# Performance work log

Measured on AMD Instinct MI355X. Metric: run time of the kernel, lower is better.

Reference implementation:

```python
import jax, jax.numpy as jnp
import numpy as np

N_NODES = 100000
N_EDGES = 3200000
EPS = 1e-5
NEG_SLOPE = 0.1


def _glorot(key, fan_in, fan_out):
    lim = np.sqrt(6.0 / (fan_in + fan_out))
    return jax.random.uniform(key, (fan_in, fan_out), jnp.float32, -lim, lim)


def setup_inputs() -> dict:
    key = jax.random.key(0)
    ks = jax.random.split(key, 16)
    x = jax.random.normal(ks[0], (N_NODES, 3), jnp.float32)
    edge_index = jax.random.randint(ks[1], (2, N_EDGES), 0, N_NODES, jnp.int32)
    dims = [(3, 64), (64, 64), (64, 256), (256, 256), (256, 512), (512, 1)]
    inp = {"x": x, "edge_index": edge_index}
    for i, (fi, fo) in enumerate(dims):
        inp[f"W{i+1}"] = _glorot(ks[2 + i], fi, fo)
        inp[f"b{i+1}"] = jnp.zeros((fo,), jnp.float32)
    for i, fo in enumerate([64, 64, 256, 256, 512]):
        inp[f"g{i+1}"] = jnp.ones((fo,), jnp.float32)
        inp[f"bt{i+1}"] = jnp.zeros((fo,), jnp.float32)
    return inp


def _gcn_conv(h, W, b, src, dst, dis):
    # transform first (cheaper when out_dim <= in_dim is not guaranteed, but
    # avoids gathering raw features twice); then edge-normalized scatter-add.
    hw = h @ W                                   # [N, Fo]
    norm = dis[src] * dis[dst]                   # [E]
    agg = jax.ops.segment_sum(hw[src] * norm[:, None], dst, num_segments=N_NODES)
    agg = agg + (dis * dis)[:, None] * hw        # self-loop term (norm = dis_i^2)
    return agg + b


def _bn(h, g, bt):
    mu = jnp.mean(h, axis=0)
    var = jnp.mean((h - mu) ** 2, axis=0)        # biased var, as torch BN
    return (h - mu) * jax.lax.rsqrt(var + EPS) * g + bt


def _lrelu(h):
    return jnp.where(h > 0, h, NEG_SLOPE * h)


def reference(x, edge_index, W1, b1, W2, b2, W3, b3, W4, b4, W5, b5, W6, b6,
              g1, bt1, g2, bt2, g3, bt3, g4, bt4, g5, bt5):
    src, dst = edge_index[0], edge_index[1]
    # degree includes the added self-loop (+1), symmetric normalization
    deg = jax.ops.segment_sum(jnp.ones((N_EDGES,), x.dtype), dst,
                              num_segments=N_NODES) + 1.0
    dis = jax.lax.rsqrt(deg)

    h = x
    Ws = [W1, W2, W3, W4, W5]
    bs = [b1, b2, b3, b4, b5]
    gs = [g1, g2, g3, g4, g5]
    bts = [bt1, bt2, bt3, bt4, bt5]
    for W, b, g, bt in zip(Ws, bs, gs, bts):
        h = _gcn_conv(h, W, b, src, dst, dis)
        h = _lrelu(_bn(h, g, bt))
    h = _gcn_conv(h, W6, b6, src, dst, dis)
    return jax.nn.sigmoid(h)
```

## Files before the change

kernel.cpp:

```cpp
#include <hip/hip_runtime.h>
#include <math.h>

typedef unsigned short u16;
typedef unsigned int u32;
typedef __attribute__((ext_vector_type(8))) short bf16x8;
typedef __attribute__((ext_vector_type(4))) float f32x4;

constexpr float EPS_BN = 1e-5f;
constexpr float NEG = 0.1f;
constexpr int LDP = 800;

static inline int cdiv(int a, int b) { return (a + b - 1) / b; }


__device__ __forceinline__ float b2f_lo(u32 v) { return __uint_as_float(v << 16); }
__device__ __forceinline__ float b2f_hi(u32 v) { return __uint_as_float(v & 0xFFFF0000u); }
__device__ __forceinline__ float b2f(u16 v) { return __uint_as_float(((u32)v) << 16); }
__device__ __forceinline__ u16 f2b(float f) {
  u32 u = __float_as_uint(f);
  u32 r = u + 0x7FFFu + ((u >> 16) & 1u);
  return (u16)(r >> 16);
}
__device__ __forceinline__ u32 pack2(float a, float b) {
  return (u32)f2b(a) | ((u32)f2b(b) << 16);
}
__device__ __forceinline__ void unpack8(uint4 v, float* o) {
  o[0] = b2f_lo(v.x); o[1] = b2f_hi(v.x);
  o[2] = b2f_lo(v.y); o[3] = b2f_hi(v.y);
  o[4] = b2f_lo(v.z); o[5] = b2f_hi(v.z);
  o[6] = b2f_lo(v.w); o[7] = b2f_hi(v.w);
}
__device__ __forceinline__ void unpack4(uint2 v, float* o) {
  o[0] = b2f_lo(v.x); o[1] = b2f_hi(v.x);
  o[2] = b2f_lo(v.y); o[3] = b2f_hi(v.y);
}


__global__ void k_zero_i32(int* p, int n) {
  int i = blockIdx.x * blockDim.x + threadIdx.x;
  if (i < n) p[i] = 0;
}

__global__ __launch_bounds__(256) void k_bcount(const int* __restrict__ dst,
                                                int* __restrict__ bucketCnt, int E) {
  __shared__ int hist[256];
  int tid = threadIdx.x;
  hist[tid] = 0;
  __syncthreads();
  int e0 = blockIdx.x * 4096;
#pragma unroll
  for (int i = 0; i < 16; ++i) {
    int e = e0 + i * 256 + tid;
    if (e < E) atomicAdd(&hist[dst[e] >> 9], 1);
  }
  __syncthreads();
  int h = hist[tid];
  if (h > 0) atomicAdd(&bucketCnt[tid], h);
}

__global__ void k_bscan(const int* __restrict__ bucketCnt, int* __restrict__ bucketOff,
                        int* __restrict__ bucketCur, int NB, int E) {
  __shared__ int s[256];
  int tid = threadIdx.x;
  int v = (tid < NB) ? bucketCnt[tid] : 0;
  s[tid] = v;
  __syncthreads();
  for (int off = 1; off < 256; off <<= 1) {
    int t = (tid >= off) ? s[tid - off] : 0;
    __syncthreads();
    s[tid] += t;
    __syncthreads();
  }
  if (tid < NB) bucketOff[tid] = s[tid] - v;
  if (tid == NB) bucketOff[NB] = E;
  if (tid < NB) bucketCur[tid] = 0;
}

__global__ __launch_bounds__(256) void k_bucket(const int* __restrict__ src,
                                                const int* __restrict__ dst,
                                                const int* __restrict__ bucketOff,
                                                int* __restrict__ bucketCur,
                                                u32* __restrict__ ebuf, int E) {
  __shared__ int hist[256];
  __shared__ int base[256];
  __shared__ int lcur[256];
  int tid = threadIdx.x;
  hist[tid] = 0; lcur[tid] = 0;
  __syncthreads();
  int e0 = blockIdx.x * 4096;
  int ss[16], dd[16];
#pragma unroll
  for (int i = 0; i < 16; ++i) {
    int e = e0 + i * 256 + tid;
    if (e < E) {
      ss[i] = src[e]; dd[i] = dst[e];
      atomicAdd(&hist[dd[i] >> 9], 1);
    } else dd[i] = -1;
  }
  __syncthreads();
  int h = hist[tid];
  if (h > 0) base[tid] = bucketOff[tid] + atomicAdd(&bucketCur[tid], h);
  __syncthreads();
#pragma unroll
  for (int i = 0; i < 16; ++i) {
    if (dd[i] >= 0) {
      int bk = dd[i] >> 9;
      int p = atomicAdd(&lcur[bk], 1);
      ebuf[base[bk] + p] = ((u32)ss[i] << 9) | ((u32)dd[i] & 511u);
    }
  }
}

__global__ __launch_bounds__(256) void k_csr(const u32* __restrict__ ebuf,
                                             const int* __restrict__ bucketOff,
                                             int* __restrict__ rowoff,
                                             int* __restrict__ col,
                                             float* __restrict__ dis,
                                             int N, int E, int NB) {
  __shared__ int hist[512];
  __shared__ int loff[512];
  __shared__ int scan_s[256];
  int b = blockIdx.x;
  int tid = threadIdx.x;
  int ebase = bucketOff[b], eend = bucketOff[b + 1];
  int ecnt = eend - ebase;
  hist[tid] = 0; hist[tid + 256] = 0;
  __syncthreads();
  for (int i = tid; i < ecnt; i += 256)
    atomicAdd(&hist[ebuf[ebase + i] & 511u], 1);
  __syncthreads();
  int h0 = hist[2 * tid], h1 = hist[2 * tid + 1];
  int ts = h0 + h1;
  scan_s[tid] = ts;
  __syncthreads();
  for (int off = 1; off < 256; off <<= 1) {
    int t = (tid >= off) ? scan_s[tid - off] : 0;
    __syncthreads();
    scan_s[tid] += t;
    __syncthreads();
  }
  int excl = scan_s[tid] - ts;
  loff[2 * tid] = excl;
  loff[2 * tid + 1] = excl + h0;
  __syncthreads();
  int gbase = b * 512;
  for (int i = tid; i < 512; i += 256) {
    int node = gbase + i;
    if (node < N) {
      rowoff[node] = ebase + loff[i];
      dis[node] = rsqrtf((float)hist[i] + 1.0f);
    }
  }
  if (b == NB - 1 && tid == 0) rowoff[N] = E;
  __syncthreads();
  for (int i = tid; i < ecnt; i += 256) {
    u32 ed = ebuf[ebase + i];
    int p = atomicAdd(&loff[ed & 511u], 1);
    col[ebase + p] = (int)(ed >> 9);
  }
}


__global__ void k_l1(const float* __restrict__ x, const int* __restrict__ rowoff,
                     const int* __restrict__ col, const float* __restrict__ dis,
                     const float* __restrict__ W, const float* __restrict__ b,
                     u16* __restrict__ z, int n) {
  int wid = (blockIdx.x * blockDim.x + threadIdx.x) >> 6;
  int lane = threadIdx.x & 63;
  if (wid >= n) return;
  float a0 = 0.f, a1 = 0.f, a2 = 0.f;
  int beg = rowoff[wid], end = rowoff[wid + 1];
  for (int e = beg + lane; e < end; e += 64) {
    int j = col[e];
    float dj = dis[j];
    a0 += dj * x[j * 3 + 0];
    a1 += dj * x[j * 3 + 1];
    a2 += dj * x[j * 3 + 2];
  }
#pragma unroll
  for (int off = 32; off; off >>= 1) {
    a0 += __shfl_xor(a0, off); a1 += __shfl_xor(a1, off); a2 += __shfl_xor(a2, off);
  }
  float di = dis[wid];
  a0 = di * (a0 + di * x[wid * 3 + 0]);
  a1 = di * (a1 + di * x[wid * 3 + 1]);
  a2 = di * (a2 + di * x[wid * 3 + 2]);
  float zv = a0 * W[lane] + a1 * W[64 + lane] + a2 * W[128 + lane] + b[lane];
  z[(size_t)wid * 64 + lane] = f2b(zv);
}


__global__ void k_agg64(const u16* __restrict__ u, const int* __restrict__ rowoff,
                        const int* __restrict__ col, const float* __restrict__ dis,
                        u16* __restrict__ a, int n) {
  int wid = (blockIdx.x * blockDim.x + threadIdx.x) >> 6;
  int lane = threadIdx.x & 63;
  if (wid >= n) return;
  int sub = lane >> 4, c = lane & 15;
  const uint2* u2 = (const uint2*)u;
  float acc[4] = {0.f, 0.f, 0.f, 0.f};
  if (sub == 0) {
    float s[4]; unpack4(u2[(size_t)wid * 16 + c], s);
#pragma unroll
    for (int k = 0; k < 4; ++k) acc[k] = s[k];
  }
  int beg = rowoff[wid], end = rowoff[wid + 1];
  int e = beg + sub;
  int j1 = (e < end) ? col[e] : -1;
  int j2 = (e + 4 < end) ? col[e + 4] : -1;
  while (j1 >= 0) {
    int en = e + 8;
    int nj1 = -1, nj2 = -1;
    if (j2 >= 0) {
      if (en < end) nj1 = col[en];
      if (en + 4 < end) nj2 = col[en + 4];
    }
    {
      float f1[4]; unpack4(u2[(size_t)j1 * 16 + c], f1);
#pragma unroll
      for (int k = 0; k < 4; ++k) acc[k] += f1[k];
    }
    if (j2 >= 0) {
      float f2[4]; unpack4(u2[(size_t)j2 * 16 + c], f2);
#pragma unroll
      for (int k = 0; k < 4; ++k) acc[k] += f2[k];
    }
    e = en; j1 = nj1; j2 = nj2;
  }
#pragma unroll
  for (int k = 0; k < 4; ++k) {
    acc[k] += __shfl_xor(acc[k], 16);
    acc[k] += __shfl_xor(acc[k], 32);
  }
  if (sub == 0) {
    float d = dis[wid];
    ((uint2*)a)[(size_t)wid * 16 + c] =
        make_uint2(pack2(d * acc[0], d * acc[1]), pack2(d * acc[2], d * acc[3]));
  }
}

__global__ void k_agg256(const u16* __restrict__ u, const int* __restrict__ rowoff,
                         const int* __restrict__ col, const float* __restrict__ dis,
                         u16* __restrict__ a, int n) {
  int wid = (blockIdx.x * blockDim.x + threadIdx.x) >> 6;
  int lane = threadIdx.x & 63;
  if (wid >= n) return;
  int sub = lane >> 5, c = lane & 31;
  const uint4* u4 = (const uint4*)u;
  float acc[8] = {0.f, 0.f, 0.f, 0.f, 0.f, 0.f, 0.f, 0.f};
  if (sub == 0) {
    float s[8]; unpack8(u4[(size_t)wid * 32 + c], s);
#pragma unroll
    for (int k = 0; k < 8; ++k) acc[k] = s[k];
  }
  int beg = rowoff[wid], end = rowoff[wid + 1];
  int e = beg + sub;
  int j1 = (e < end) ? col[e] : -1;
  int j2 = (e + 2 < end) ? col[e + 2] : -1;
  while (j1 >= 0) {
    int en = e + 4;
    int nj1 = -1, nj2 = -1;
    if (j2 >= 0) {
      if (en < end) nj1 = col[en];
      if (en + 2 < end) nj2 = col[en + 2];
    }
    {
      float f1[8]; unpack8(u4[(size_t)j1 * 32 + c], f1);
#pragma unroll
      for (int k = 0; k < 8; ++k) acc[k] += f1[k];
    }
    if (j2 >= 0) {
      float f2[8]; unpack8(u4[(size_t)j2 * 32 + c], f2);
#pragma unroll
      for (int k = 0; k < 8; ++k) acc[k] += f2[k];
    }
    e = en; j1 = nj1; j2 = nj2;
  }
#pragma unroll
  for (int k = 0; k < 8; ++k) acc[k] += __shfl_xor(acc[k], 32);
  if (sub == 0) {
    float d = dis[wid];
    uint4 r;
    r.x = pack2(d * acc[0], d * acc[1]);
    r.y = pack2(d * acc[2], d * acc[3]);
    r.z = pack2(d * acc[4], d * acc[5]);
    r.w = pack2(d * acc[6], d * acc[7]);
    ((uint4*)a)[(size_t)wid * 32 + c] = r;
  }
}


__global__ void k_u(u16* __restrict__ z, const float* __restrict__ scaleF,
                    const float* __restrict__ shiftF, const float* __restrict__ dis,
                    int n, int lg) {
  size_t idx = (size_t)blockIdx.x * blockDim.x + threadIdx.x;
  size_t tot = ((size_t)n) << lg;
  if (idx >= tot) return;
  int g = (int)(idx & ((1u << lg) - 1));
  int node = (int)(idx >> lg);
  uint4 v = ((const uint4*)z)[idx];
  float f[8];
  unpack8(v, f);
  int f0 = g * 8;
  float4 s0 = *(const float4*)&scaleF[f0];
  float4 s1 = *(const float4*)&scaleF[f0 + 4];
  float4 h0 = *(const float4*)&shiftF[f0];
  float4 h1 = *(const float4*)&shiftF[f0 + 4];
  float d = dis[node];
  float o[8];
  o[0] = f[0] * s0.x + h0.x; o[1] = f[1] * s0.y + h0.y;
  o[2] = f[2] * s0.z + h0.z; o[3] = f[3] * s0.w + h0.w;
  o[4] = f[4] * s1.x + h1.x; o[5] = f[5] * s1.y + h1.y;
  o[6] = f[6] * s1.z + h1.z; o[7] = f[7] * s1.w + h1.w;
#pragma unroll
  for (int k = 0; k < 8; ++k) {
    float a = o[k];
    a = (a > 0.f) ? a : NEG * a;
    o[k] = d * a;
  }
  uint4 r;
  r.x = pack2(o[0], o[1]); r.y = pack2(o[2], o[3]);
  r.z = pack2(o[4], o[5]); r.w = pack2(o[6], o[7]);
  ((uint4*)z)[idx] = r;
}


__global__ void k_wt_all(const float* __restrict__ W2, const float* __restrict__ W3,
                         const float* __restrict__ W4, const float* __restrict__ W5,
                         u16* __restrict__ WT) {
  int i = blockIdx.x * blockDim.x + threadIdx.x;
  const float* W; int K, Fo, base;
  if (i < 4096)        { W = W2; K = 64;  Fo = 64;  base = 0; }
  else if (i < 20480)  { W = W3; K = 64;  Fo = 256; base = 4096; }
  else if (i < 86016)  { W = W4; K = 256; Fo = 256; base = 20480; }
  else if (i < 217088) { W = W5; K = 256; Fo = 512; base = 86016; }
  else return;
  int idx = i - base;
  int f = idx / K, k = idx - f * K;
  WT[i] = f2b(W[(size_t)k * Fo + f]);
}


__global__ __launch_bounds__(256) void k_gemm(const u16* __restrict__ A,
                                              const u16* __restrict__ WT,
                                              const float* __restrict__ bias,
                                              u16* __restrict__ C,
                                              float* __restrict__ psum,
                                              float* __restrict__ psq,
                                              int n, int K, int Fo, int nby) {
  __shared__ u16 As[128][72];
  __shared__ u16 Bs[128][72];
  int tid = threadIdx.x;
  int nwg = gridDim.x;
  int bid = blockIdx.x;
  int q = nwg >> 3, rr = nwg & 7;
  int xcd = bid & 7, pos = bid >> 3;
  int wgid = (xcd < rr ? xcd * (q + 1) : rr * (q + 1) + (xcd - rr) * q) + pos;
  int bx = wgid / nby, by = wgid - bx * nby;
  int bm0 = bx * 128, bn0 = by * 128;
  int lane = tid & 63, wid = tid >> 6;
  int wm = wid >> 1, wn = wid & 1;
  int lr = tid & 127;
  int lh = (tid >> 7) * 32;
  int fr = lane & 15, fg = lane >> 4;
  f32x4 acc[4][4];
#pragma unroll
  for (int i = 0; i < 4; ++i)
#pragma unroll
    for (int j = 0; j < 4; ++j) acc[i][j] = (f32x4)0.0f;

  for (int kt = 0; kt < K; kt += 64) {
    {
      int row = bm0 + lr;
      uint4 v[4];
#pragma unroll
      for (int i = 0; i < 4; ++i) {
        v[i] = make_uint4(0u, 0u, 0u, 0u);
        if (row < n) v[i] = *(const uint4*)&A[(size_t)row * K + kt + lh + i * 8];
      }
      int fo = bn0 + lr;
      uint4 w[4];
#pragma unroll
      for (int i = 0; i < 4; ++i) {
        w[i] = make_uint4(0u, 0u, 0u, 0u);
        if (fo < Fo) w[i] = *(const uint4*)&WT[(size_t)fo * K + kt + lh + i * 8];
      }
#pragma unroll
      for (int i = 0; i < 4; ++i) *(uint4*)&As[lr][lh + i * 8] = v[i];
#pragma unroll
      for (int i = 0; i < 4; ++i) *(uint4*)&Bs[lr][lh + i * 8] = w[i];
    }
    __syncthreads();
#pragma unroll
    for (int ks = 0; ks < 2; ++ks) {
      int k0 = ks * 32 + fg * 8;
      bf16x8 af[4], bf[4];
#pragma unroll
      for (int mi = 0; mi < 4; ++mi) af[mi] = *(const bf16x8*)&As[wm * 64 + mi * 16 + fr][k0];
#pragma unroll
      for (int ni = 0; ni < 4; ++ni) bf[ni] = *(const bf16x8*)&Bs[wn * 64 + ni * 16 + fr][k0];
#pragma unroll
      for (int mi = 0; mi < 4; ++mi)
#pragma unroll
        for (int ni = 0; ni < 4; ++ni)
          acc[mi][ni] = __builtin_amdgcn_mfma_f32_16x16x32_bf16(af[mi], bf[ni], acc[mi][ni], 0, 0, 0);
    }
    __syncthreads();
  }
  float* s2 = (float*)&As[0][0];
#pragma unroll
  for (int ni = 0; ni < 4; ++ni) {
    int gc = bn0 + wn * 64 + ni * 16 + fr;
    float ps = 0.f, pq = 0.f;
    if (gc < Fo) {
      float bv = bias[gc];
#pragma unroll
      for (int mi = 0; mi < 4; ++mi) {
#pragma unroll
        for (int rg = 0; rg < 4; ++rg) {
          int gr = bm0 + wm * 64 + mi * 16 + fg * 4 + rg;
          if (gr < n) {
            float v = acc[mi][ni][rg] + bv;
            C[(size_t)gr * Fo + gc] = f2b(v);
            ps += v; pq += v * v;
          }
        }
      }
    }
    ps += __shfl_xor(ps, 16); ps += __shfl_xor(ps, 32);
    pq += __shfl_xor(pq, 16); pq += __shfl_xor(pq, 32);
    if (fg == 0 && gc < Fo) {
      int cl = wn * 64 + ni * 16 + fr;
      s2[wm * 128 + cl] = ps;
      s2[256 + wm * 128 + cl] = pq;
    }
  }
  __syncthreads();
  if (tid < 128) {
    int gc = bn0 + tid;
    if (gc < Fo) {
      psum[(size_t)gc * LDP + bx] = s2[tid] + s2[128 + tid];
      psq[(size_t)gc * LDP + bx] = s2[256 + tid] + s2[384 + tid];
    }
  }
}


__global__ void k_colred(const u16* __restrict__ z, int Fo, int n, int rowsPerChunk,
                         float* __restrict__ psum, float* __restrict__ psq) {
  int fl = threadIdx.x & 63;
  int rg = threadIdx.x >> 6;
  int f = blockIdx.y * 64 + fl;
  int r0 = blockIdx.x * rowsPerChunk;
  int r1 = min(n, r0 + rowsPerChunk);
  float s = 0.f, sq = 0.f;
  for (int r = r0 + rg; r < r1; r += 4) {
    float v = b2f(z[(size_t)r * Fo + f]);
    s += v;
    sq += v * v;
  }
  __shared__ float ls[4][64], lq[4][64];
  ls[rg][fl] = s; lq[rg][fl] = sq;
  __syncthreads();
  if (rg == 0) {
    psum[(size_t)f * LDP + blockIdx.x] = ls[0][fl] + ls[1][fl] + ls[2][fl] + ls[3][fl];
    psq[(size_t)f * LDP + blockIdx.x] = lq[0][fl] + lq[1][fl] + lq[2][fl] + lq[3][fl];
  }
}

__global__ void k_bnparams(const float* __restrict__ psum, const float* __restrict__ psq,
                           int Fo, int nChunks, int n,
                           const float* __restrict__ g, const float* __restrict__ bt,
                           float* __restrict__ scaleF, float* __restrict__ shiftF) {
  int f = blockIdx.x * 4 + (threadIdx.x >> 6);
  int lane = threadIdx.x & 63;
  if (f >= Fo) return;
  float s = 0.f, sq = 0.f;
  const float* ps = &psum[(size_t)f * LDP];
  const float* pq = &psq[(size_t)f * LDP];
  for (int c = lane; c < nChunks; c += 64) { s += ps[c]; sq += pq[c]; }
#pragma unroll
  for (int off = 32; off; off >>= 1) {
    s += __shfl_xor(s, off);
    sq += __shfl_xor(sq, off);
  }
  if (lane == 0) {
    float inv = 1.0f / (float)n;
    float mu = s * inv;
    float var = sq * inv - mu * mu;
    float rs = rsqrtf(var + EPS_BN) * g[f];
    scaleF[f] = rs;
    shiftF[f] = bt[f] - mu * rs;
  }
}


__global__ void k_dot512(const u16* __restrict__ z, const float* __restrict__ scaleF,
                         const float* __restrict__ shiftF, const float* __restrict__ w6,
                         const float* __restrict__ dis, float* __restrict__ v, int n) {
  __shared__ float ws[512], scs[512], shs[512];
  int tid = threadIdx.x;
  for (int i = tid; i < 512; i += 256) { ws[i] = w6[i]; scs[i] = scaleF[i]; shs[i] = shiftF[i]; }
  __syncthreads();
  int lane = tid % 64, wv = tid / 64;
  int node = blockIdx.x * 4 + wv;
  if (node >= n) return;
  uint4 vz = *(const uint4*)&z[(size_t)node * 512 + lane * 8];
  float f[8];
  unpack8(vz, f);
  int f0 = lane * 8;
  float s = 0.f;
#pragma unroll
  for (int k = 0; k < 8; ++k) {
    float a = f[k] * scs[f0 + k] + shs[f0 + k];
    a = (a > 0.f) ? a : NEG * a;
    s += a * ws[f0 + k];
  }
#pragma unroll
  for (int off = 32; off > 0; off >>= 1) s += __shfl_down(s, off);
  if (lane == 0) v[node] = dis[node] * s;
}

__global__ void k_final(const float* __restrict__ v, const int* __restrict__ rowoff,
                        const int* __restrict__ col, const float* __restrict__ dis,
                        const float* __restrict__ b6, float* __restrict__ out, int n) {
  int wid = (blockIdx.x * blockDim.x + threadIdx.x) >> 6;
  int lane = threadIdx.x & 63;
  if (wid >= n) return;
  float acc = 0.f;
  int beg = rowoff[wid], end = rowoff[wid + 1];
  for (int e = beg + lane; e < end; e += 64) acc += v[col[e]];
#pragma unroll
  for (int off = 32; off; off >>= 1) acc += __shfl_xor(acc, off);
  if (lane == 0) {
    float zz = dis[wid] * (acc + v[wid]) + b6[0];
    out[wid] = 1.0f / (1.0f + expf(-zz));
  }
}


extern "C" void kernel_launch(void* const* d_in, const int* in_sizes, int n_in,
                              void* d_out, int out_size, void* d_ws, size_t ws_size,
                              hipStream_t stream) {
  const float* x = (const float*)d_in[0];
  const int* ei = (const int*)d_in[1];
  const int N = in_sizes[0] / 3;
  const int E = in_sizes[1] / 2;
  const int* srcIdx = ei;
  const int* dstIdx = ei + E;

  const float* W[6]; const float* b[6];
  for (int i = 0; i < 6; ++i) { W[i] = (const float*)d_in[2 + 2 * i]; b[i] = (const float*)d_in[3 + 2 * i]; }
  const float* g[5]; const float* bt[5];
  for (int i = 0; i < 5; ++i) { g[i] = (const float*)d_in[14 + 2 * i]; bt[i] = (const float*)d_in[15 + 2 * i]; }

  char* wsB = (char*)d_ws;
  size_t off = 0;
  auto alloc = [&](size_t bytes) -> void* {
    void* p = wsB + off;
    off = (off + bytes + 255) & ~(size_t)255;
    return p;
  };

  const int NB = cdiv(N, 512);
  int* rowoff = (int*)alloc((size_t)(N + 1) * 4);
  int* col = (int*)alloc((size_t)E * 4);
  float* dis = (float*)alloc((size_t)N * 4);
  float* vbuf = (float*)alloc((size_t)N * 4);
  float* scaleF = (float*)alloc(512 * 4);
  float* shiftF = (float*)alloc(512 * 4);
  u16* WTb = (u16*)alloc((size_t)217088 * 2);
  int* bucketCnt = (int*)alloc(256 * 4);
  int* bucketOff = (int*)alloc(257 * 4);
  int* bucketCur = (int*)alloc(256 * 4);
  const int nbx = cdiv(N, 128);
  float* psum = (float*)alloc((size_t)512 * LDP * 4);
  float* psq = (float*)alloc((size_t)512 * LDP * 4);
  u16* Zb = (u16*)alloc((size_t)N * 512 * 2);
  u16* Ab = (u16*)alloc((size_t)N * 256 * 2);
  u32* ebuf = (u32*)Ab;

  const int wtOff[5] = {0, 0, 4096, 20480, 86016};
  k_wt_all<<<cdiv(217088, 256), 256, 0, stream>>>(W[1], W[2], W[3], W[4], WTb);

  const int EB = cdiv(E, 4096);
  k_zero_i32<<<1, 256, 0, stream>>>(bucketCnt, 256);
  k_bcount<<<EB, 256, 0, stream>>>(dstIdx, bucketCnt, E);
  k_bscan<<<1, 256, 0, stream>>>(bucketCnt, bucketOff, bucketCur, NB, E);
  k_bucket<<<EB, 256, 0, stream>>>(srcIdx, dstIdx, bucketOff, bucketCur, ebuf, E);
  k_csr<<<NB, 256, 0, stream>>>(ebuf, bucketOff, rowoff, col, dis, N, E, NB);

  auto gemm = [&](const u16* Ain, int layer, int K, int Fo, u16* Cout) {
    int nby = cdiv(Fo, 128);
    k_gemm<<<nbx * nby, 256, 0, stream>>>(Ain, WTb + wtOff[layer], b[layer], Cout,
                                          psum, psq, N, K, Fo, nby);
    k_bnparams<<<cdiv(Fo, 4), 256, 0, stream>>>(psum, psq, Fo, nbx, N,
                                                g[layer], bt[layer], scaleF, shiftF);
  };

  const int waveGrid = cdiv(N * 64, 256);

  k_l1<<<waveGrid, 256, 0, stream>>>(x, rowoff, col, dis, W[0], b[0], Zb, N);
  {
    const int rowsPerChunk = 2048;
    const int nChunks = cdiv(N, rowsPerChunk);
    dim3 grid(nChunks, 1);
    k_colred<<<grid, 256, 0, stream>>>(Zb, 64, N, rowsPerChunk, psum, psq);
    k_bnparams<<<cdiv(64, 4), 256, 0, stream>>>(psum, psq, 64, nChunks, N, g[0], bt[0], scaleF, shiftF);
  }

  k_u<<<cdiv(N * 8, 256), 256, 0, stream>>>(Zb, scaleF, shiftF, dis, N, 3);
  k_agg64<<<waveGrid, 256, 0, stream>>>(Zb, rowoff, col, dis, Ab, N);
  gemm(Ab, 1, 64, 64, Zb);

  k_u<<<cdiv(N * 8, 256), 256, 0, stream>>>(Zb, scaleF, shiftF, dis, N, 3);
  k_agg64<<<waveGrid, 256, 0, stream>>>(Zb, rowoff, col, dis, Ab, N);
  gemm(Ab, 2, 64, 256, Zb);

  k_u<<<cdiv(N * 32, 256), 256, 0, stream>>>(Zb, scaleF, shiftF, dis, N, 5);
  k_agg256<<<waveGrid, 256, 0, stream>>>(Zb, rowoff, col, dis, Ab, N);
  gemm(Ab, 3, 256, 256, Zb);

  k_u<<<cdiv(N * 32, 256), 256, 0, stream>>>(Zb, scaleF, shiftF, dis, N, 5);
  k_agg256<<<waveGrid, 256, 0, stream>>>(Zb, rowoff, col, dis, Ab, N);
  gemm(Ab, 4, 256, 512, Zb);

  k_dot512<<<cdiv(N, 4), 256, 0, stream>>>(Zb, scaleF, shiftF, W[5], dis, vbuf, N);
  k_final<<<waveGrid, 256, 0, stream>>>(vbuf, rowoff, col, dis, b[5], (float*)d_out, N);
}
```

Measured before the change: 1.235 ms.

## Fuse BN+LeakyReLU into aggregation and use direct-to-LDS swizzled GEMM loads

```diff
diff --git a/kernel.cpp b/kernel.cpp
--- a/kernel.cpp
+++ b/kernel.cpp
@@ -33,6 +33,13 @@
 __device__ __forceinline__ void unpack4(uint2 v, float* o) {
   o[0] = b2f_lo(v.x); o[1] = b2f_hi(v.x);
   o[2] = b2f_lo(v.y); o[3] = b2f_hi(v.y);
+}
+__device__ __forceinline__ float lrelu_s(float t) { return fmaxf(t, NEG * t); }
+
+__device__ __forceinline__ void gload16(const void* g, void* l) {
+  __builtin_amdgcn_global_load_lds(
+      (const __attribute__((address_space(1))) u32*)g,
+      (__attribute__((address_space(3))) u32*)l, 16, 0, 0);
 }
 
 
@@ -190,24 +197,29 @@
 }
 
 
-__global__ void k_agg64(const u16* __restrict__ u, const int* __restrict__ rowoff,
+__global__ void k_agg64(const u16* __restrict__ z, const int* __restrict__ rowoff,
                         const int* __restrict__ col, const float* __restrict__ dis,
+                        const float* __restrict__ scaleF, const float* __restrict__ shiftF,
                         u16* __restrict__ a, int n) {
   int wid = (blockIdx.x * blockDim.x + threadIdx.x) >> 6;
   int lane = threadIdx.x & 63;
   if (wid >= n) return;
   int sub = lane >> 4, c = lane & 15;
-  const uint2* u2 = (const uint2*)u;
+  const uint2* z2 = (const uint2*)z;
+  float sc[4], sh[4];
+  {
+    float4 s = *(const float4*)&scaleF[c * 4];
+    float4 h = *(const float4*)&shiftF[c * 4];
+    sc[0] = s.x; sc[1] = s.y; sc[2] = s.z; sc[3] = s.w;
+    sh[0] = h.x; sh[1] = h.y; sh[2] = h.z; sh[3] = h.w;
+  }
   float acc[4] = {0.f, 0.f, 0.f, 0.f};
-  if (sub == 0) {
-    float s[4]; unpack4(u2[(size_t)wid * 16 + c], s);
-#pragma unroll
-    for (int k = 0; k < 4; ++k) acc[k] = s[k];
-  }
   int beg = rowoff[wid], end = rowoff[wid + 1];
   int e = beg + sub;
   int j1 = (e < end) ? col[e] : -1;
   int j2 = (e + 4 < end) ? col[e + 4] : -1;
+  float d1 = (j1 >= 0) ? dis[j1] : 0.f;
+  float d2 = (j2 >= 0) ? dis[j2] : 0.f;
   while (j1 >= 0) {
     int en = e + 8;
     int nj1 = -1, nj2 = -1;
@@ -215,17 +227,19 @@
       if (en < end) nj1 = col[en];
       if (en + 4 < end) nj2 = col[en + 4];
     }
+    float nd1 = (nj1 >= 0) ? dis[nj1] : 0.f;
+    float nd2 = (nj2 >= 0) ? dis[nj2] : 0.f;
     {
-      float f1[4]; unpack4(u2[(size_t)j1 * 16 + c], f1);
-#pragma unroll
-      for (int k = 0; k < 4; ++k) acc[k] += f1[k];
+      float f1[4]; unpack4(z2[(size_t)j1 * 16 + c], f1);
+#pragma unroll
+      for (int k = 0; k < 4; ++k) acc[k] += lrelu_s(d1 * (f1[k] * sc[k] + sh[k]));
     }
     if (j2 >= 0) {
-      float f2[4]; unpack4(u2[(size_t)j2 * 16 + c], f2);
-#pragma unroll
-      for (int k = 0; k < 4; ++k) acc[k] += f2[k];
-    }
-    e = en; j1 = nj1; j2 = nj2;
+      float f2[4]; unpack4(z2[(size_t)j2 * 16 + c], f2);
+#pragma unroll
+      for (int k = 0; k < 4; ++k) acc[k] += lrelu_s(d2 * (f2[k] * sc[k] + sh[k]));
+    }
+    e = en; j1 = nj1; j2 = nj2; d1 = nd1; d2 = nd2;
   }
 #pragma unroll
   for (int k = 0; k < 4; ++k) {
@@ -233,30 +247,42 @@
     acc[k] += __shfl_xor(acc[k], 32);
   }
   if (sub == 0) {
-    float d = dis[wid];
+    float dw = dis[wid];
+    float s[4]; unpack4(z2[(size_t)wid * 16 + c], s);
+#pragma unroll
+    for (int k = 0; k < 4; ++k) acc[k] = dw * (acc[k] + lrelu_s(dw * (s[k] * sc[k] + sh[k])));
     ((uint2*)a)[(size_t)wid * 16 + c] =
-        make_uint2(pack2(d * acc[0], d * acc[1]), pack2(d * acc[2], d * acc[3]));
-  }
-}
-
-__global__ void k_agg256(const u16* __restrict__ u, const int* __restrict__ rowoff,
+        make_uint2(pack2(acc[0], acc[1]), pack2(acc[2], acc[3]));
+  }
+}
+
+__global__ void k_agg256(const u16* __restrict__ z, const int* __restrict__ rowoff,
                          const int* __restrict__ col, const float* __restrict__ dis,
+                         const float* __restrict__ scaleF, const float* __restrict__ shiftF,
                          u16* __restrict__ a, int n) {
   int wid = (blockIdx.x * blockDim.x + threadIdx.x) >> 6;
   int lane = threadIdx.x & 63;
   if (wid >= n) return;
   int sub = lane >> 5, c = lane & 31;
-  const uint4* u4 = (const uint4*)u;
+  const uint4* z4 = (const uint4*)z;
+  float sc[8], sh[8];
+  {
+    float4 s0 = *(const float4*)&scaleF[c * 8];
+    float4 s1 = *(const float4*)&scaleF[c * 8 + 4];
+    float4 h0 = *(const float4*)&shiftF[c * 8];
+    float4 h1 = *(const float4*)&shiftF[c * 8 + 4];
+    sc[0] = s0.x; sc[1] = s0.y; sc[2] = s0.z; sc[3] = s0.w;
+    sc[4] = s1.x; sc[5] = s1.y; sc[6] = s1.z; sc[7] = s1.w;
+    sh[0] = h0.x; sh[1] = h0.y; sh[2] = h0.z; sh[3] = h0.w;
+    sh[4] = h1.x; sh[5] = h1.y; sh[6] = h1.z; sh[7] = h1.w;
+  }
   float acc[8] = {0.f, 0.f, 0.f, 0.f, 0.f, 0.f, 0.f, 0.f};
-  if (sub == 0) {
-    float s[8]; unpack8(u4[(size_t)wid * 32 + c], s);
-#pragma unroll
-    for (int k = 0; k < 8; ++k) acc[k] = s[k];
-  }
   int beg = rowoff[wid], end = rowoff[wid + 1];
   int e = beg + sub;
   int j1 = (e < end) ? col[e] : -1;
   int j2 = (e + 2 < end) ? col[e + 2] : -1;
+  float d1 = (j1 >= 0) ? dis[j1] : 0.f;
+  float d2 = (j2 >= 0) ? dis[j2] : 0.f;
   while (j1 >= 0) {
     int en = e + 4;
     int nj1 = -1, nj2 = -1;
@@ -264,64 +290,34 @@
       if (en < end) nj1 = col[en];
       if (en + 2 < end) nj2 = col[en + 2];
     }
+    float nd1 = (nj1 >= 0) ? dis[nj1] : 0.f;
+    float nd2 = (nj2 >= 0) ? dis[nj2] : 0.f;
     {
-      float f1[8]; unpack8(u4[(size_t)j1 * 32 + c], f1);
-#pragma unroll
-      for (int k = 0; k < 8; ++k) acc[k] += f1[k];
+      float f1[8]; unpack8(z4[(size_t)j1 * 32 + c], f1);
+#pragma unroll
+      for (int k = 0; k < 8; ++k) acc[k] += lrelu_s(d1 * (f1[k] * sc[k] + sh[k]));
     }
     if (j2 >= 0) {
-      float f2[8]; unpack8(u4[(size_t)j2 * 32 + c], f2);
-#pragma unroll
-      for (int k = 0; k < 8; ++k) acc[k] += f2[k];
-    }
-    e = en; j1 = nj1; j2 = nj2;
+      float f2[8]; unpack8(z4[(size_t)j2 * 32 + c], f2);
+#pragma unroll
+      for (int k = 0; k < 8; ++k) acc[k] += lrelu_s(d2 * (f2[k] * sc[k] + sh[k]));
+    }
+    e = en; j1 = nj1; j2 = nj2; d1 = nd1; d2 = nd2;
   }
 #pragma unroll
   for (int k = 0; k < 8; ++k) acc[k] += __shfl_xor(acc[k], 32);
   if (sub == 0) {
-    float d = dis[wid];
+    float dw = dis[wid];
+    float s[8]; unpack8(z4[(size_t)wid * 32 + c], s);
+#pragma unroll
+    for (int k = 0; k < 8; ++k) acc[k] = dw * (acc[k] + lrelu_s(dw * (s[k] * sc[k] + sh[k])));
     uint4 r;
-    r.x = pack2(d * acc[0], d * acc[1]);
-    r.y = pack2(d * acc[2], d * acc[3]);
-    r.z = pack2(d * acc[4], d * acc[5]);
-    r.w = pack2(d * acc[6], d * acc[7]);
+    r.x = pack2(acc[0], acc[1]);
+    r.y = pack2(acc[2], acc[3]);
+    r.z = pack2(acc[4], acc[5]);
+    r.w = pack2(acc[6], acc[7]);
     ((uint4*)a)[(size_t)wid * 32 + c] = r;
   }
-}
-
-
-__global__ void k_u(u16* __restrict__ z, const float* __restrict__ scaleF,
-                    const float* __restrict__ shiftF, const float* __restrict__ dis,
-                    int n, int lg) {
-  size_t idx = (size_t)blockIdx.x * blockDim.x + threadIdx.x;
-  size_t tot = ((size_t)n) << lg;
-  if (idx >= tot) return;
-  int g = (int)(idx & ((1u << lg) - 1));
-  int node = (int)(idx >> lg);
-  uint4 v = ((const uint4*)z)[idx];
-  float f[8];
-  unpack8(v, f);
-  int f0 = g * 8;
-  float4 s0 = *(const float4*)&scaleF[f0];
-  float4 s1 = *(const float4*)&scaleF[f0 + 4];
-  float4 h0 = *(const float4*)&shiftF[f0];
-  float4 h1 = *(const float4*)&shiftF[f0 + 4];
-  float d = dis[node];
-  float o[8];
-  o[0] = f[0] * s0.x + h0.x; o[1] = f[1] * s0.y + h0.y;
-  o[2] = f[2] * s0.z + h0.z; o[3] = f[3] * s0.w + h0.w;
-  o[4] = f[4] * s1.x + h1.x; o[5] = f[5] * s1.y + h1.y;
-  o[6] = f[6] * s1.z + h1.z; o[7] = f[7] * s1.w + h1.w;
-#pragma unroll
-  for (int k = 0; k < 8; ++k) {
-    float a = o[k];
-    a = (a > 0.f) ? a : NEG * a;
-    o[k] = d * a;
-  }
-  uint4 r;
-  r.x = pack2(o[0], o[1]); r.y = pack2(o[2], o[3]);
-  r.z = pack2(o[4], o[5]); r.w = pack2(o[6], o[7]);
-  ((uint4*)z)[idx] = r;
 }
 
 
@@ -348,8 +344,8 @@
                                               float* __restrict__ psum,
                                               float* __restrict__ psq,
                                               int n, int K, int Fo, int nby) {
-  __shared__ u16 As[128][72];
-  __shared__ u16 Bs[128][72];
+  __shared__ u16 As[128 * 64];
+  __shared__ u16 Bs[128 * 64];
   int tid = threadIdx.x;
   int nwg = gridDim.x;
   int bid = blockIdx.x;
@@ -358,11 +354,11 @@
   int wgid = (xcd < rr ? xcd * (q + 1) : rr * (q + 1) + (xcd - rr) * q) + pos;
   int bx = wgid / nby, by = wgid - bx * nby;
   int bm0 = bx * 128, bn0 = by * 128;
-  int lane = tid & 63, wid = tid >> 6;
-  int wm = wid >> 1, wn = wid & 1;
-  int lr = tid & 127;
-  int lh = (tid >> 7) * 32;
+  int lane = tid & 63, wv = tid >> 6;
+  int wm = wv >> 1, wn = wv & 1;
   int fr = lane & 15, fg = lane >> 4;
+  int srow = lane >> 3;
+  int cb = (lane & 7) ^ srow;
   f32x4 acc[4][4];
 #pragma unroll
   for (int i = 0; i < 4; ++i)
@@ -370,25 +366,13 @@
     for (int j = 0; j < 4; ++j) acc[i][j] = (f32x4)0.0f;
 
   for (int kt = 0; kt < K; kt += 64) {
-    {
-      int row = bm0 + lr;
-      uint4 v[4];
-#pragma unroll
-      for (int i = 0; i < 4; ++i) {
-        v[i] = make_uint4(0u, 0u, 0u, 0u);
-        if (row < n) v[i] = *(const uint4*)&A[(size_t)row * K + kt + lh + i * 8];
-      }
-      int fo = bn0 + lr;
-      uint4 w[4];
-#pragma unroll
-      for (int i = 0; i < 4; ++i) {
-        w[i] = make_uint4(0u, 0u, 0u, 0u);
-        if (fo < Fo) w[i] = *(const uint4*)&WT[(size_t)fo * K + kt + lh + i * 8];
-      }
-#pragma unroll
-      for (int i = 0; i < 4; ++i) *(uint4*)&As[lr][lh + i * 8] = v[i];
-#pragma unroll
-      for (int i = 0; i < 4; ++i) *(uint4*)&Bs[lr][lh + i * 8] = w[i];
+#pragma unroll
+    for (int i = 0; i < 4; ++i) {
+      int rb = 8 * (4 * wv + i);
+      const u16* ga = &A[(size_t)(bm0 + rb + srow) * K + kt + cb * 8];
+      gload16(ga, &As[rb * 64 + lane * 8]);
+      const u16* gb = &WT[(size_t)(bn0 + rb + srow) * K + kt + cb * 8];
+      gload16(gb, &Bs[rb * 64 + lane * 8]);
     }
     __syncthreads();
 #pragma unroll
@@ -396,9 +380,17 @@
       int k0 = ks * 32 + fg * 8;
       bf16x8 af[4], bf[4];
 #pragma unroll
-      for (int mi = 0; mi < 4; ++mi) af[mi] = *(const bf16x8*)&As[wm * 64 + mi * 16 + fr][k0];
-#pragma unroll
-      for (int ni = 0; ni < 4; ++ni) bf[ni] = *(const bf16x8*)&Bs[wn * 64 + ni * 16 + fr][k0];
+      for (int mi = 0; mi < 4; ++mi) {
+        int row = wm * 64 + mi * 16 + fr;
+        int byt = (row * 128 + k0 * 2) ^ ((row & 7) << 4);
+        af[mi] = *(const bf16x8*)((const char*)As + byt);
+      }
+#pragma unroll
+      for (int ni = 0; ni < 4; ++ni) {
+        int row = wn * 64 + ni * 16 + fr;
+        int byt = (row * 128 + k0 * 2) ^ ((row & 7) << 4);
+        bf[ni] = *(const bf16x8*)((const char*)Bs + byt);
+      }
 #pragma unroll
       for (int mi = 0; mi < 4; ++mi)
 #pragma unroll
@@ -407,7 +399,7 @@
     }
     __syncthreads();
   }
-  float* s2 = (float*)&As[0][0];
+  float* s2 = (float*)&As[0];
 #pragma unroll
   for (int ni = 0; ni < 4; ++ni) {
     int gc = bn0 + wn * 64 + ni * 16 + fr;
@@ -577,7 +569,7 @@
   float* psum = (float*)alloc((size_t)512 * LDP * 4);
   float* psq = (float*)alloc((size_t)512 * LDP * 4);
   u16* Zb = (u16*)alloc((size_t)N * 512 * 2);
-  u16* Ab = (u16*)alloc((size_t)N * 256 * 2);
+  u16* Ab = (u16*)alloc((size_t)(N + 128) * 256 * 2);
   u32* ebuf = (u32*)Ab;
 
   const int wtOff[5] = {0, 0, 4096, 20480, 86016};
@@ -609,20 +601,16 @@
     k_bnparams<<<cdiv(64, 4), 256, 0, stream>>>(psum, psq, 64, nChunks, N, g[0], bt[0], scaleF, shiftF);
   }
 
-  k_u<<<cdiv(N * 8, 256), 256, 0, stream>>>(Zb, scaleF, shiftF, dis, N, 3);
-  k_agg64<<<waveGrid, 256, 0, stream>>>(Zb, rowoff, col, dis, Ab, N);
+  k_agg64<<<waveGrid, 256, 0, stream>>>(Zb, rowoff, col, dis, scaleF, shiftF, Ab, N);
   gemm(Ab, 1, 64, 64, Zb);
 
-  k_u<<<cdiv(N * 8, 256), 256, 0, stream>>>(Zb, scaleF, shiftF, dis, N, 3);
-  k_agg64<<<waveGrid, 256, 0, stream>>>(Zb, rowoff, col, dis, Ab, N);
+  k_agg64<<<waveGrid, 256, 0, stream>>>(Zb, rowoff, col, dis, scaleF, shiftF, Ab, N);
   gemm(Ab, 2, 64, 256, Zb);
 
-  k_u<<<cdiv(N * 32, 256), 256, 0, stream>>>(Zb, scaleF, shiftF, dis, N, 5);
-  k_agg256<<<waveGrid, 256, 0, stream>>>(Zb, rowoff, col, dis, Ab, N);
+  k_agg256<<<waveGrid, 256, 0, stream>>>(Zb, rowoff, col, dis, scaleF, shiftF, Ab, N);
   gemm(Ab, 3, 256, 256, Zb);
 
-  k_u<<<cdiv(N * 32, 256), 256, 0, stream>>>(Zb, scaleF, shiftF, dis, N, 5);
-  k_agg256<<<waveGrid, 256, 0, stream>>>(Zb, rowoff, col, dis, Ab, N);
+  k_agg256<<<waveGrid, 256, 0, stream>>>(Zb, rowoff, col, dis, scaleF, shiftF, Ab, N);
   gemm(Ab, 4, 256, 512, Zb);
 
   k_dot512<<<cdiv(N, 4), 256, 0, stream>>>(Zb, scaleF, shiftF, W[5], dis, vbuf, N);
```

Result: faster. 1.205 ms (-2.4%).
